# Kernel optimization log

Measured on AMD Instinct MI355X. Metric: run time of the kernel, lower is better.

The kernel has to match this reference:

```python
import jax, jax.numpy as jnp
import numpy as np

N_THRESH = 100  # thresholds = 0.00, 0.01, ..., 0.99


def setup_inputs() -> dict:
    key = jax.random.key(0)
    k1, k2 = jax.random.split(key)
    predicted_mask = jax.random.uniform(k1, (32, 1, 1024, 1024), dtype=jnp.float32)
    gt_mask = jax.random.randint(k2, (32, 1, 1024, 1024), 0, 2, dtype=jnp.int32)
    return {"predicted_mask": predicted_mask, "gt_mask": gt_mask}


def reference(predicted_mask, gt_mask):
    # Single-pass histogram formulation of: for each t_k in arange(0,1,0.01),
    # iou_k = |(pred > t_k) & gt| / |(pred > t_k) | gt|  (torchmetrics binary Jaccard,
    # strict '>' thresholding, safe-divide -> 0 when union is empty).
    thresholds = jnp.arange(0.0, 1.0, 0.01, dtype=jnp.float32)  # [100], sorted
    pred = jnp.squeeze(predicted_mask).ravel()                  # [N] probabilities in [0,1]
    gt = jnp.squeeze(gt_mask).ravel().astype(jnp.float32)       # [N] 0/1

    # cnt[i] = number of thresholds strictly below pred[i]; pixel i satisfies
    # (pred > t_k) exactly for k in [0, cnt[i]).
    cnt = jnp.searchsorted(thresholds, pred, side='left')       # [N] int in [0, 100]

    hist_pos = jax.ops.segment_sum(gt, cnt, num_segments=N_THRESH + 1)              # [101]
    hist_all = jax.ops.segment_sum(jnp.ones_like(gt), cnt, num_segments=N_THRESH + 1)

    # TP_k = #{pred > t_k and gt==1} = sum_{c > k} hist_pos[c]  (suffix sums via cumsum)
    tp = jnp.sum(hist_pos) - jnp.cumsum(hist_pos)[:N_THRESH]        # [100]
    pred_pos = jnp.sum(hist_all) - jnp.cumsum(hist_all)[:N_THRESH]  # [100] #{pred > t_k}
    n_gt_pos = jnp.sum(gt)

    union = pred_pos + n_gt_pos - tp                                 # TP + FP + FN
    ious = jnp.where(union > 0, tp / jnp.maximum(union, 1.0), 0.0)   # safe divide -> 0
    return thresholds, ious
```

## Files before the change

kernel.cpp:

```cpp
#include <hip/hip_runtime.h>
#include <stdint.h>

#define N_THRESH 100
#define NBINS 101
#define NWORDS 51

__global__ void zero_ws_kernel(unsigned long long* __restrict__ ws) {
    int i = threadIdx.x;
    if (i < NBINS) ws[i] = 0ull;
}

__device__ __forceinline__ int bin_of(float v) {
    int e = (int)(v * 100.0f);
    e = e < 0 ? 0 : (e > 99 ? 99 : e);
    double ed = (double)e * 0.01;
    float t0 = (float)ed;
    float t1 = (float)(ed + 0.01);
    int c = e + (t0 < v ? 1 : 0) + (t1 < v ? 1 : 0);
    return c > N_THRESH ? N_THRESH : c;
}

__global__ __launch_bounds__(256) void hist_kernel(
        const float* __restrict__ pred,
        const int* __restrict__ gt,
        unsigned long long* __restrict__ ws,
        int n) {
    __shared__ uint32_t hist[4][NWORDS][64];
    __shared__ uint32_t pcnt[NBINS], ppos[NBINS];

    const int tid  = threadIdx.x;
    const int wave = tid >> 6;
    const int lane = tid & 63;

    for (int i = lane; i < NWORDS * 64; i += 64) (&hist[wave][0][0])[i] = 0u;
    if (tid < NBINS) { pcnt[tid] = 0u; ppos[tid] = 0u; }

    const int nvec = n >> 2;
    const float4* __restrict__ p4 = (const float4*)pred;
    const int4*   __restrict__ g4 = (const int4*)gt;
    const int gsz = gridDim.x * blockDim.x;

    int i = blockIdx.x * blockDim.x + tid;
    if (i < nvec) {
        float4 p = p4[i];
        int4   g = g4[i];
        for (int j = i + gsz; j < nvec; j += gsz) {
            float4 pn = p4[j];
            int4   gn = g4[j];
            int c0 = bin_of(p.x), c1 = bin_of(p.y);
            int c2 = bin_of(p.z), c3 = bin_of(p.w);
            hist[wave][c0 >> 1][lane] +=
                (1u | ((uint32_t)(g.x != 0) << 8)) << ((c0 & 1) * 16);
            hist[wave][c1 >> 1][lane] +=
                (1u | ((uint32_t)(g.y != 0) << 8)) << ((c1 & 1) * 16);
            hist[wave][c2 >> 1][lane] +=
                (1u | ((uint32_t)(g.z != 0) << 8)) << ((c2 & 1) * 16);
            hist[wave][c3 >> 1][lane] +=
                (1u | ((uint32_t)(g.w != 0) << 8)) << ((c3 & 1) * 16);
            p = pn; g = gn;
        }
        int c0 = bin_of(p.x), c1 = bin_of(p.y);
        int c2 = bin_of(p.z), c3 = bin_of(p.w);
        hist[wave][c0 >> 1][lane] +=
            (1u | ((uint32_t)(g.x != 0) << 8)) << ((c0 & 1) * 16);
        hist[wave][c1 >> 1][lane] +=
            (1u | ((uint32_t)(g.y != 0) << 8)) << ((c1 & 1) * 16);
        hist[wave][c2 >> 1][lane] +=
            (1u | ((uint32_t)(g.z != 0) << 8)) << ((c2 & 1) * 16);
        hist[wave][c3 >> 1][lane] +=
            (1u | ((uint32_t)(g.w != 0) << 8)) << ((c3 & 1) * 16);
    }

    if (blockIdx.x == 0 && tid == 0) {
        for (int k = nvec << 2; k < n; ++k) {
            int c = bin_of(pred[k]);
            hist[0][c >> 1][0] +=
                (1u | ((uint32_t)(gt[k] != 0) << 8)) << ((c & 1) * 16);
        }
    }

    __syncthreads();
    if (lane < NWORDS) {
        uint32_t c0 = 0, p0 = 0, c1 = 0, p1 = 0;
        for (int c = 0; c < 64; ++c) {
            uint32_t v = hist[wave][lane][(c + lane) & 63];
            c0 += v & 0xffu;         p0 += (v >> 8) & 0xffu;
            c1 += (v >> 16) & 0xffu; p1 += v >> 24;
        }
        const int b0 = lane * 2, b1 = lane * 2 + 1;
        atomicAdd(&pcnt[b0], c0);
        atomicAdd(&ppos[b0], p0);
        if (b1 < NBINS) {
            atomicAdd(&pcnt[b1], c1);
            atomicAdd(&ppos[b1], p1);
        }
    }
    __syncthreads();

    if (tid < NBINS) {
        unsigned long long s =
            ((unsigned long long)ppos[tid] << 32) | (unsigned long long)pcnt[tid];
        if (s) atomicAdd(&ws[tid], s);
    }
}

__global__ void finalize_kernel(const unsigned long long* __restrict__ ws,
                                float* __restrict__ out) {
    __shared__ unsigned int pos[NBINS], all[NBINS];
    int k = threadIdx.x;
    if (k < NBINS) {
        unsigned long long h = ws[k];
        pos[k] = (unsigned int)(h >> 32);
        all[k] = (unsigned int)(h & 0xffffffffull);
    }
    __syncthreads();
    if (k < N_THRESH) {
        out[k] = (float)((double)k * 0.01);
        unsigned long long tp = 0, pp = 0, ngt = 0;
        for (int c = k + 1; c <= N_THRESH; ++c) { tp += pos[c]; pp += all[c]; }
        for (int c = 0; c <= N_THRESH; ++c) ngt += pos[c];
        long long uni = (long long)(pp + ngt - tp);
        double iou = (uni > 0) ? (double)tp / (double)uni : 0.0;
        out[N_THRESH + k] = (float)iou;
    }
}

extern "C" void kernel_launch(void* const* d_in, const int* in_sizes, int n_in,
                              void* d_out, int out_size, void* d_ws, size_t ws_size,
                              hipStream_t stream) {
    const float* pred = (const float*)d_in[0];
    const int*   gt   = (const int*)d_in[1];
    float* out = (float*)d_out;
    unsigned long long* ws = (unsigned long long*)d_ws;
    int n = in_sizes[0];

    zero_ws_kernel<<<1, 128, 0, stream>>>(ws);
    int grid = 768;
    int need = (n + 51199) / 51200;
    if (need > grid) grid = need;
    hist_kernel<<<grid, 256, 0, stream>>>(pred, gt, ws, n);
    finalize_kernel<<<1, 128, 0, stream>>>(ws, out);
}
```

Before: 285.9 us.

## Batch eight vector loads per thread and offload some bins to global atomics

The grid-stride loop becomes a super-iteration that issues eight float4/int4 loads up front to raise memory-level parallelism. Five of the eight vectors go to the per-wave LDS histogram and three go through 64-bit global atomics into 64 sliced histograms in workspace, so the work is split between the LDS and L2 atomic paths. The grid grows from 768 to 2048 blocks, and the zero and finalize kernels now clear and sum the extra slots. Global atomics on only 101 bins per slot may contend heavily, and the workspace must be larger than before.

After: 634.9 us. 2.22x slower.

```diff
diff --git a/kernel.cpp b/kernel.cpp
--- a/kernel.cpp
+++ b/kernel.cpp
@@ -4,10 +4,12 @@
 #define N_THRESH 100
 #define NBINS 101
 #define NWORDS 51
+#define NSLOT 64
+#define SLOT_OFF NBINS
 
 __global__ void zero_ws_kernel(unsigned long long* __restrict__ ws) {
-    int i = threadIdx.x;
-    if (i < NBINS) ws[i] = 0ull;
+    int i = blockIdx.x * blockDim.x + threadIdx.x;
+    if (i < NBINS + NSLOT * NBINS) ws[i] = 0ull;
 }
 
 __device__ __forceinline__ int bin_of(float v) {
@@ -39,26 +41,49 @@
     const float4* __restrict__ p4 = (const float4*)pred;
     const int4*   __restrict__ g4 = (const int4*)gt;
     const int gsz = gridDim.x * blockDim.x;
+    const int t   = blockIdx.x * blockDim.x + tid;
+    unsigned long long* __restrict__ slot =
+        ws + SLOT_OFF + (blockIdx.x & (NSLOT - 1)) * NBINS;
 
-    int i = blockIdx.x * blockDim.x + tid;
-    if (i < nvec) {
+    const int nsuper = nvec / (8 * gsz);
+    for (int s = 0; s < nsuper; ++s) {
+        const int base = s * 8 * gsz + t;
+        float4 p[8];
+        int4   g[8];
+#pragma unroll
+        for (int k = 0; k < 8; ++k) {
+            p[k] = p4[base + k * gsz];
+            g[k] = g4[base + k * gsz];
+        }
+#pragma unroll
+        for (int k = 0; k < 5; ++k) {
+            int c0 = bin_of(p[k].x), c1 = bin_of(p[k].y);
+            int c2 = bin_of(p[k].z), c3 = bin_of(p[k].w);
+            hist[wave][c0 >> 1][lane] +=
+                (1u | ((uint32_t)(g[k].x != 0) << 8)) << ((c0 & 1) * 16);
+            hist[wave][c1 >> 1][lane] +=
+                (1u | ((uint32_t)(g[k].y != 0) << 8)) << ((c1 & 1) * 16);
+            hist[wave][c2 >> 1][lane] +=
+                (1u | ((uint32_t)(g[k].z != 0) << 8)) << ((c2 & 1) * 16);
+            hist[wave][c3 >> 1][lane] +=
+                (1u | ((uint32_t)(g[k].w != 0) << 8)) << ((c3 & 1) * 16);
+        }
+#pragma unroll
+        for (int k = 5; k < 8; ++k) {
+            atomicAdd(&slot[bin_of(p[k].x)],
+                      1ull | ((unsigned long long)(g[k].x != 0) << 32));
+            atomicAdd(&slot[bin_of(p[k].y)],
+                      1ull | ((unsigned long long)(g[k].y != 0) << 32));
+            atomicAdd(&slot[bin_of(p[k].z)],
+                      1ull | ((unsigned long long)(g[k].z != 0) << 32));
+            atomicAdd(&slot[bin_of(p[k].w)],
+                      1ull | ((unsigned long long)(g[k].w != 0) << 32));
+        }
+    }
+
+    for (int i = nsuper * 8 * gsz + t; i < nvec; i += gsz) {
         float4 p = p4[i];
         int4   g = g4[i];
-        for (int j = i + gsz; j < nvec; j += gsz) {
-            float4 pn = p4[j];
-            int4   gn = g4[j];
-            int c0 = bin_of(p.x), c1 = bin_of(p.y);
-            int c2 = bin_of(p.z), c3 = bin_of(p.w);
-            hist[wave][c0 >> 1][lane] +=
-                (1u | ((uint32_t)(g.x != 0) << 8)) << ((c0 & 1) * 16);
-            hist[wave][c1 >> 1][lane] +=
-                (1u | ((uint32_t)(g.y != 0) << 8)) << ((c1 & 1) * 16);
-            hist[wave][c2 >> 1][lane] +=
-                (1u | ((uint32_t)(g.z != 0) << 8)) << ((c2 & 1) * 16);
-            hist[wave][c3 >> 1][lane] +=
-                (1u | ((uint32_t)(g.w != 0) << 8)) << ((c3 & 1) * 16);
-            p = pn; g = gn;
-        }
         int c0 = bin_of(p.x), c1 = bin_of(p.y);
         int c2 = bin_of(p.z), c3 = bin_of(p.w);
         hist[wave][c0 >> 1][lane] +=
@@ -106,12 +131,18 @@
 
 __global__ void finalize_kernel(const unsigned long long* __restrict__ ws,
                                 float* __restrict__ out) {
-    __shared__ unsigned int pos[NBINS], all[NBINS];
+    __shared__ unsigned long long pos[NBINS], all[NBINS];
     int k = threadIdx.x;
     if (k < NBINS) {
         unsigned long long h = ws[k];
-        pos[k] = (unsigned int)(h >> 32);
-        all[k] = (unsigned int)(h & 0xffffffffull);
+        unsigned long long p = h >> 32, c = h & 0xffffffffull;
+        for (int s = 0; s < NSLOT; ++s) {
+            unsigned long long v = ws[SLOT_OFF + s * NBINS + k];
+            p += v >> 32;
+            c += v & 0xffffffffull;
+        }
+        pos[k] = p;
+        all[k] = c;
     }
     __syncthreads();
     if (k < N_THRESH) {
@@ -134,9 +165,10 @@
     unsigned long long* ws = (unsigned long long*)d_ws;
     int n = in_sizes[0];
 
-    zero_ws_kernel<<<1, 128, 0, stream>>>(ws);
-    int grid = 768;
-    int need = (n + 51199) / 51200;
+    zero_ws_kernel<<<26, 256, 0, stream>>>(ws);
+    int nvec = n >> 2;
+    int grid = 2048;
+    int need = (nvec + 4095) / 4096;
     if (need > grid) grid = need;
     hist_kernel<<<grid, 256, 0, stream>>>(pred, gt, ws, n);
     finalize_kernel<<<1, 128, 0, stream>>>(ws, out);
```
